# Kernel optimization log

Hardware: AMD Instinct MI355X
Metric: run time of the kernel (lower is better)

The kernel has to match this reference:

```python
import jax, jax.numpy as jnp
import numpy as np

N_NODES = 100000
N_EDGES = 1600000
NFEAT = 512
HIDDEN = 128
NCLASS = 40


def setup_inputs() -> dict:
    key = jax.random.key(0)
    ks = jax.random.split(key, 8)
    x = jax.random.normal(ks[0], (N_NODES, NFEAT), dtype=jnp.float32)
    edge_src = jax.random.randint(ks[1], (N_EDGES,), 0, N_NODES, dtype=jnp.int32)
    edge_dst = jax.random.randint(ks[2], (N_EDGES,), 0, N_NODES, dtype=jnp.int32)
    # normalized adjacency values (D^-1/2 A D^-1/2 style), all positive
    edge_val = jax.random.uniform(ks[3], (N_EDGES,), dtype=jnp.float32)
    # glorot-ish init like pygcn's reset_parameters
    W1 = jax.random.normal(ks[4], (NFEAT, HIDDEN), dtype=jnp.float32) / np.sqrt(NFEAT)
    b1 = jnp.zeros((HIDDEN,), dtype=jnp.float32)
    W2 = jax.random.normal(ks[5], (HIDDEN, NCLASS), dtype=jnp.float32) / np.sqrt(HIDDEN)
    b2 = jnp.zeros((NCLASS,), dtype=jnp.float32)
    return {"x": x, "edge_src": edge_src, "edge_dst": edge_dst, "edge_val": edge_val,
            "W1": W1, "b1": b1, "W2": W2, "b2": b2}


def _gcn_layer(h, edge_src, edge_dst, edge_val, W, b):
    # support = h @ W ; out = spmm(adj, support) + b
    support = h @ W                                  # [N, d_out]
    msg = support[edge_src] * edge_val[:, None]      # [E, d_out] gather
    agg = jax.ops.segment_sum(msg, edge_dst, num_segments=N_NODES)  # scatter-add
    return agg + b


def reference(x, edge_src, edge_dst, edge_val, W1, b1, W2, b2):
    h = _gcn_layer(x, edge_src, edge_dst, edge_val, W1, b1)
    h = jax.nn.relu(h)
    # dropout=0.0 -> branch skipped (faithful to `if self.dropout:` with falsy value)
    h = _gcn_layer(h, edge_src, edge_dst, edge_val, W2, b2)
    return jax.nn.log_softmax(h, axis=1)
```

## Files before the change

kernel.cpp:

```cpp
#include <hip/hip_runtime.h>
#include <stdint.h>

#define NN 100000
#define NE 1600000
#define NF 512
#define NH 128
#define NC 40
#define BKT 64

typedef float f32x4 __attribute__((ext_vector_type(4)));
typedef short bf16x8 __attribute__((ext_vector_type(8)));

__device__ __forceinline__ unsigned short f2bf(float f){
    unsigned u = __float_as_uint(f);
    u = u + 0x7FFFu + ((u >> 16) & 1u);
    return (unsigned short)(u >> 16);
}
__device__ __forceinline__ unsigned pk2(float a, float b){
    return (unsigned)f2bf(a) | ((unsigned)f2bf(b) << 16);
}
__device__ __forceinline__ float blo(unsigned u){ return __uint_as_float(u << 16); }
__device__ __forceinline__ float bhi(unsigned u){ return __uint_as_float(u & 0xffff0000u); }

__global__ __launch_bounds__(256) void edge_prep(const int* __restrict__ esrc,
                       const int* __restrict__ edst, const float* __restrict__ eval,
                       int* __restrict__ deg, int2* __restrict__ pk,
                       const float* __restrict__ W1, const float* __restrict__ W2,
                       unsigned short* __restrict__ W1t, unsigned short* __restrict__ W2t){
    if (blockIdx.x < 280){
        int tid = blockIdx.x * 256 + threadIdx.x;
        if (tid < NF * NH){
            int c = tid >> 9;
            int k = tid & 511;
            W1t[c * NF + k] = f2bf(W1[k * NH + c]);
        }
        int t2 = tid - NF * NH;
        if (t2 >= 0 && t2 < 48 * NH){
            int c = t2 >> 7;
            int k = t2 & 127;
            W2t[c * NH + k] = (c < NC) ? f2bf(W2[k * NC + c]) : (unsigned short)0;
        }
    } else {
        int tid = (blockIdx.x - 280) * 256 + threadIdx.x;
        if (tid < NE){
            int d = edst[tid];
            int pos = atomicAdd(&deg[d], 1);
            if (pos < BKT)
                pk[(size_t)d * BKT + pos] = make_int2(esrc[tid], __float_as_int(eval[tid]));
        }
    }
}

__global__ __launch_bounds__(256, 3) void gemm1(const float* __restrict__ x,
                                                const unsigned short* __restrict__ W1t,
                                                unsigned short* __restrict__ s1){
    __shared__ unsigned short Al[2][128 * 40];
    __shared__ unsigned short Bl[2][128 * 40];
    const int tid  = threadIdx.x;
    const int wid  = tid >> 6;
    const int lane = tid & 63;
    const int quad = lane >> 4;
    const int l15  = lane & 15;
    const int br   = blockIdx.x * 128;

    const int r    = tid >> 1;
    const int half = tid & 1;

    int arow = br + r; if (arow >= NN) arow = NN - 1;
    const float* aptr = x + (size_t)arow * NF + half * 16;
    const unsigned short* bptr = W1t + (size_t)r * NF + half * 16;

    float4 pa0, pa1, pa2, pa3;
    uint4  pb0, pb1;
    {
        const float4* ap = (const float4*)aptr;
        pa0 = ap[0]; pa1 = ap[1]; pa2 = ap[2]; pa3 = ap[3];
        const uint4* bp = (const uint4*)bptr;
        pb0 = bp[0]; pb1 = bp[1];
        unsigned* Ad = (unsigned*)&Al[0][r * 40 + half * 16];
        Ad[0] = pk2(pa0.x, pa0.y); Ad[1] = pk2(pa0.z, pa0.w);
        Ad[2] = pk2(pa1.x, pa1.y); Ad[3] = pk2(pa1.z, pa1.w);
        Ad[4] = pk2(pa2.x, pa2.y); Ad[5] = pk2(pa2.z, pa2.w);
        Ad[6] = pk2(pa3.x, pa3.y); Ad[7] = pk2(pa3.z, pa3.w);
        uint4* Bd = (uint4*)&Bl[0][r * 40 + half * 16];
        Bd[0] = pb0; Bd[1] = pb1;
    }
    __syncthreads();

    f32x4 acc[2][8];
#pragma unroll
    for (int i = 0; i < 2; i++)
#pragma unroll
        for (int j = 0; j < 8; j++) acc[i][j] = (f32x4){0.f, 0.f, 0.f, 0.f};

    int cur = 0;
    for (int ks = 0; ks < NF; ks += 32){
        const bool more = (ks + 32 < NF);
        if (more){
            const float4* ap = (const float4*)(aptr + ks + 32);
            pa0 = ap[0]; pa1 = ap[1]; pa2 = ap[2]; pa3 = ap[3];
            const uint4* bp = (const uint4*)(bptr + ks + 32);
            pb0 = bp[0]; pb1 = bp[1];
        }

        bf16x8 a0 = *(const bf16x8*)&Al[cur][(wid * 32 +      l15) * 40 + quad * 8];
        bf16x8 a1 = *(const bf16x8*)&Al[cur][(wid * 32 + 16 + l15) * 40 + quad * 8];
        bf16x8 bb[8];
#pragma unroll
        for (int ct = 0; ct < 8; ct++)
            bb[ct] = *(const bf16x8*)&Bl[cur][(ct * 16 + l15) * 40 + quad * 8];
#pragma unroll
        for (int ct = 0; ct < 8; ct++){
            acc[0][ct] = __builtin_amdgcn_mfma_f32_16x16x32_bf16(a0, bb[ct], acc[0][ct], 0, 0, 0);
            acc[1][ct] = __builtin_amdgcn_mfma_f32_16x16x32_bf16(a1, bb[ct], acc[1][ct], 0, 0, 0);
        }

        if (more){
            int nxt = cur ^ 1;
            unsigned* Ad = (unsigned*)&Al[nxt][r * 40 + half * 16];
            Ad[0] = pk2(pa0.x, pa0.y); Ad[1] = pk2(pa0.z, pa0.w);
            Ad[2] = pk2(pa1.x, pa1.y); Ad[3] = pk2(pa1.z, pa1.w);
            Ad[4] = pk2(pa2.x, pa2.y); Ad[5] = pk2(pa2.z, pa2.w);
            Ad[6] = pk2(pa3.x, pa3.y); Ad[7] = pk2(pa3.z, pa3.w);
            uint4* Bd = (uint4*)&Bl[nxt][r * 40 + half * 16];
            Bd[0] = pb0; Bd[1] = pb1;
        }
        __syncthreads();
        cur ^= 1;
    }

#pragma unroll
    for (int rt = 0; rt < 2; rt++)
#pragma unroll
        for (int ct = 0; ct < 8; ct++)
#pragma unroll
            for (int i = 0; i < 4; i++){
                int row = br + wid * 32 + rt * 16 + quad * 4 + i;
                if (row < NN) s1[(size_t)row * NH + ct * 16 + l15] = f2bf(acc[rt][ct][i]);
            }
}

__global__ __launch_bounds__(256) void agg1(const uint4* __restrict__ s1v,
                                            const int* __restrict__ deg,
                                            const int2* __restrict__ pk,
                                            const float* __restrict__ b1, uint4* __restrict__ h){
    const int lane  = threadIdx.x & 63;
    const int quad  = lane >> 4;
    const int hl    = lane & 15;
    const int lbase = quad * 16;
    const int node  = blockIdx.x * 16 + (threadIdx.x >> 6) * 4 + quad;

    const int s = node * BKT;
    int dg = deg[node]; if (dg > BKT) dg = BKT;
    const int e = s + dg;
    float a[8];
#pragma unroll
    for (int t = 0; t < 8; t++) a[t] = 0.f;

    int2 rec = make_int2(0, 0);
    {
        int c0 = e - s; if (c0 > 16) c0 = 16;
        if (hl < c0) rec = pk[s + hl];
    }
    for (int base = s; base < e; base += 16){
        int cnt = e - base; if (cnt > 16) cnt = 16;
        int2 cur = rec;
        int nb = base + 16;
        if (nb < e){
            int cn = e - nb; if (cn > 16) cn = 16;
            rec = make_int2(0, 0);
            if (hl < cn) rec = pk[nb + hl];
        }
        int j = 0;
        for (; j + 8 <= cnt; j += 8){
            int is[8];
#pragma unroll
            for (int q = 0; q < 8; q++) is[q] = __shfl(cur.x, lbase + j + q, 64);
            uint4 us[8];
#pragma unroll
            for (int q = 0; q < 8; q++) us[q] = s1v[(size_t)is[q] * 16 + hl];
            float vs[8];
#pragma unroll
            for (int q = 0; q < 8; q++) vs[q] = __int_as_float(__shfl(cur.y, lbase + j + q, 64));
#pragma unroll
            for (int q = 0; q < 8; q++){
                float v = vs[q];
                a[0] += v * blo(us[q].x); a[1] += v * bhi(us[q].x);
                a[2] += v * blo(us[q].y); a[3] += v * bhi(us[q].y);
                a[4] += v * blo(us[q].z); a[5] += v * bhi(us[q].z);
                a[6] += v * blo(us[q].w); a[7] += v * bhi(us[q].w);
            }
        }
        for (; j < cnt; j++){
            int   i0 = __shfl(cur.x, lbase + j, 64);
            float v0 = __int_as_float(__shfl(cur.y, lbase + j, 64));
            uint4 u  = s1v[(size_t)i0 * 16 + hl];
            a[0] += v0 * blo(u.x); a[1] += v0 * bhi(u.x);
            a[2] += v0 * blo(u.y); a[3] += v0 * bhi(u.y);
            a[4] += v0 * blo(u.z); a[5] += v0 * bhi(u.z);
            a[6] += v0 * blo(u.w); a[7] += v0 * bhi(u.w);
        }
    }
    const float4* b1v = (const float4*)b1;
    float4 bA = b1v[2 * hl], bB = b1v[2 * hl + 1];
    a[0] += bA.x; a[1] += bA.y; a[2] += bA.z; a[3] += bA.w;
    a[4] += bB.x; a[5] += bB.y; a[6] += bB.z; a[7] += bB.w;
#pragma unroll
    for (int t = 0; t < 8; t++) a[t] = fmaxf(a[t], 0.f);
    h[(size_t)node * 16 + hl] = make_uint4(pk2(a[0], a[1]), pk2(a[2], a[3]),
                                           pk2(a[4], a[5]), pk2(a[6], a[7]));
}

__global__ __launch_bounds__(256) void gemm2(const unsigned short* __restrict__ h,
                                             const unsigned short* __restrict__ W2t,
                                             unsigned short* __restrict__ s2p){
    const int tid  = threadIdx.x;
    const int wid  = tid >> 6;
    const int lane = tid & 63;
    const int quad = lane >> 4;
    const int l15  = lane & 15;
    const int row0 = blockIdx.x * 64 + wid * 16;

    bf16x8 bf[3][4];
#pragma unroll
    for (int ct = 0; ct < 3; ct++)
#pragma unroll
        for (int ks = 0; ks < 4; ks++)
            bf[ct][ks] = *(const bf16x8*)&W2t[(ct * 16 + l15) * NH + ks * 32 + quad * 8];

    int arow = row0 + l15; if (arow >= NN) arow = NN - 1;
    const unsigned short* ap = h + (size_t)arow * NH;

    bf16x8 a[4];
#pragma unroll
    for (int ks = 0; ks < 4; ks++) a[ks] = *(const bf16x8*)&ap[ks * 32 + quad * 8];

    f32x4 acc[3];
#pragma unroll
    for (int ct = 0; ct < 3; ct++) acc[ct] = (f32x4){0.f, 0.f, 0.f, 0.f};
#pragma unroll
    for (int ks = 0; ks < 4; ks++)
#pragma unroll
        for (int ct = 0; ct < 3; ct++)
            acc[ct] = __builtin_amdgcn_mfma_f32_16x16x32_bf16(a[ks], bf[ct][ks], acc[ct], 0, 0, 0);

#pragma unroll
    for (int ct = 0; ct < 3; ct++)
#pragma unroll
        for (int i = 0; i < 4; i++){
            int row = row0 + quad * 4 + i;
            if (row < NN) s2p[(size_t)row * 64 + ct * 16 + l15] = f2bf(acc[ct][i]);
        }
}

__global__ __launch_bounds__(256) void agg2(const uint4* __restrict__ s2v,
                                            const int* __restrict__ deg,
                                            const int2* __restrict__ pk,
                                            const float* __restrict__ b2, float* __restrict__ out){
    const int lane  = threadIdx.x & 63;
    const int oct   = lane >> 3;
    const int hl    = lane & 7;
    const int lbase = oct * 8;
    const int node  = blockIdx.x * 32 + (threadIdx.x >> 6) * 8 + oct;

    const int s = node * BKT;
    int dg = deg[node]; if (dg > BKT) dg = BKT;
    const int e = s + dg;
    float a[8];
#pragma unroll
    for (int t = 0; t < 8; t++) a[t] = 0.f;

    int2 rec = make_int2(0, 0);
    {
        int c0 = e - s; if (c0 > 8) c0 = 8;
        if (hl < c0) rec = pk[s + hl];
    }
    for (int base = s; base < e; base += 8){
        int cnt = e - base; if (cnt > 8) cnt = 8;
        int2 cur = rec;
        int nb = base + 8;
        if (nb < e){
            int cn = e - nb; if (cn > 8) cn = 8;
            rec = make_int2(0, 0);
            if (hl < cn) rec = pk[nb + hl];
        }
        if (cnt == 8){
            int is[8];
#pragma unroll
            for (int q = 0; q < 8; q++) is[q] = __shfl(cur.x, lbase + q, 64);
            uint4 us[8];
#pragma unroll
            for (int q = 0; q < 8; q++) us[q] = s2v[(size_t)is[q] * 8 + hl];
            float vs[8];
#pragma unroll
            for (int q = 0; q < 8; q++) vs[q] = __int_as_float(__shfl(cur.y, lbase + q, 64));
#pragma unroll
            for (int q = 0; q < 8; q++){
                float v = vs[q];
                a[0] += v * blo(us[q].x); a[1] += v * bhi(us[q].x);
                a[2] += v * blo(us[q].y); a[3] += v * bhi(us[q].y);
                a[4] += v * blo(us[q].z); a[5] += v * bhi(us[q].z);
                a[6] += v * blo(us[q].w); a[7] += v * bhi(us[q].w);
            }
        } else {
            for (int j = 0; j < cnt; j++){
                int   i0 = __shfl(cur.x, lbase + j, 64);
                float v0 = __int_as_float(__shfl(cur.y, lbase + j, 64));
                uint4 u  = s2v[(size_t)i0 * 8 + hl];
                a[0] += v0 * blo(u.x); a[1] += v0 * bhi(u.x);
                a[2] += v0 * blo(u.y); a[3] += v0 * bhi(u.y);
                a[4] += v0 * blo(u.z); a[5] += v0 * bhi(u.z);
                a[6] += v0 * blo(u.w); a[7] += v0 * bhi(u.w);
            }
        }
    }
    const bool act = hl < 5;
    float z[8];
    if (act){
        const float4* b2v = (const float4*)b2;
        float4 cA = b2v[2 * hl], cB = b2v[2 * hl + 1];
        z[0] = a[0] + cA.x; z[1] = a[1] + cA.y; z[2] = a[2] + cA.z; z[3] = a[3] + cA.w;
        z[4] = a[4] + cB.x; z[5] = a[5] + cB.y; z[6] = a[6] + cB.z; z[7] = a[7] + cB.w;
    } else {
#pragma unroll
        for (int t = 0; t < 8; t++) z[t] = -INFINITY;
    }
    float m = z[0];
#pragma unroll
    for (int t = 1; t < 8; t++) m = fmaxf(m, z[t]);
#pragma unroll
    for (int o = 4; o; o >>= 1) m = fmaxf(m, __shfl_xor(m, o, 8));
    float pe = 0.f;
    if (act){
#pragma unroll
        for (int t = 0; t < 8; t++) pe += __expf(z[t] - m);
    }
#pragma unroll
    for (int o = 4; o; o >>= 1) pe += __shfl_xor(pe, o, 8);
    if (act){
        float l = __logf(pe) + m;
        float* op = out + (size_t)node * NC + 8 * hl;
        *(float4*)op       = make_float4(z[0] - l, z[1] - l, z[2] - l, z[3] - l);
        *(float4*)(op + 4) = make_float4(z[4] - l, z[5] - l, z[6] - l, z[7] - l);
    }
}

extern "C" void kernel_launch(void* const* d_in, const int* in_sizes, int n_in,
                              void* d_out, int out_size, void* d_ws, size_t ws_size,
                              hipStream_t stream) {
    const float* x    = (const float*)d_in[0];
    const int*   esrc = (const int*)  d_in[1];
    const int*   edst = (const int*)  d_in[2];
    const float* eval = (const float*)d_in[3];
    const float* W1   = (const float*)d_in[4];
    const float* b1   = (const float*)d_in[5];
    const float* W2   = (const float*)d_in[6];
    const float* b2   = (const float*)d_in[7];
    float* out = (float*)d_out;

    char* ws = (char*)d_ws;
    size_t off = 0;
    auto alloc = [&](size_t bytes) -> void* {
        void* p = ws + off;
        off += (bytes + 255) & ~(size_t)255;
        return p;
    };
    unsigned short* W1t  = (unsigned short*)alloc((size_t)NF * NH * 2);
    unsigned short* W2t  = (unsigned short*)alloc((size_t)48 * NH * 2);
    unsigned short* s1   = (unsigned short*)alloc((size_t)NN * NH * 2);
    unsigned short* h    = (unsigned short*)alloc((size_t)NN * NH * 2);
    unsigned short* s2p  = (unsigned short*)alloc((size_t)NN * 64 * 2);
    int*   deg   = (int*)  alloc((size_t)NN * 4);
    int2*  pk    = (int2*) alloc((size_t)NN * BKT * 8);

    hipMemsetAsync(deg, 0, (size_t)NN * 4, stream);

    edge_prep<<<280 + (NE + 255) / 256, 256, 0, stream>>>(esrc, edst, eval, deg, pk, W1, W2, W1t, W2t);
    gemm1    <<<(NN + 127) / 128, 256, 0, stream>>>(x, W1t, s1);
    agg1     <<<NN / 16, 256, 0, stream>>>((const uint4*)s1, deg, pk, b1, (uint4*)h);
    gemm2    <<<(NN + 63) / 64, 256, 0, stream>>>(h, W2t, s2p);
    agg2     <<<NN / 32, 256, 0, stream>>>((const uint4*)s2p, deg, pk, b2, out);
}
```

Before: 551.9 us.

## Fuse edge bucketing into gemm1 launch and pad degree counters apart

Splits the weight transpose into its own small kernel and merges the edge bucketing blocks into the gemm1 launch as extra blocks, so the atomic-heavy edge scatter can overlap with the dense GEMM. Degree counters are spaced 16 ints apart (64 bytes) so that atomics to different nodes do not contend on the same cache line. In exchange the memset grows 16x (6.4 MB), agg kernels read deg with a strided pattern, and the GEMM blocks now share the device with edge blocks.

Result: faster. 501.6 us (-9.1%).

```diff
diff --git a/kernel.cpp b/kernel.cpp
--- a/kernel.cpp
+++ b/kernel.cpp
@@ -7,6 +7,8 @@
 #define NH 128
 #define NC 40
 #define BKT 64
+#define DEGS 16
+#define NGB 782
 
 typedef float f32x4 __attribute__((ext_vector_type(4)));
 typedef short bf16x8 __attribute__((ext_vector_type(8)));
@@ -22,40 +24,41 @@
 __device__ __forceinline__ float blo(unsigned u){ return __uint_as_float(u << 16); }
 __device__ __forceinline__ float bhi(unsigned u){ return __uint_as_float(u & 0xffff0000u); }
 
-__global__ __launch_bounds__(256) void edge_prep(const int* __restrict__ esrc,
-                       const int* __restrict__ edst, const float* __restrict__ eval,
-                       int* __restrict__ deg, int2* __restrict__ pk,
-                       const float* __restrict__ W1, const float* __restrict__ W2,
-                       unsigned short* __restrict__ W1t, unsigned short* __restrict__ W2t){
-    if (blockIdx.x < 280){
-        int tid = blockIdx.x * 256 + threadIdx.x;
-        if (tid < NF * NH){
-            int c = tid >> 9;
-            int k = tid & 511;
-            W1t[c * NF + k] = f2bf(W1[k * NH + c]);
-        }
-        int t2 = tid - NF * NH;
-        if (t2 >= 0 && t2 < 48 * NH){
-            int c = t2 >> 7;
-            int k = t2 & 127;
-            W2t[c * NH + k] = (c < NC) ? f2bf(W2[k * NC + c]) : (unsigned short)0;
-        }
-    } else {
-        int tid = (blockIdx.x - 280) * 256 + threadIdx.x;
+__global__ __launch_bounds__(256) void wprep(const float* __restrict__ W1, const float* __restrict__ W2,
+                                             unsigned short* __restrict__ W1t, unsigned short* __restrict__ W2t){
+    int tid = blockIdx.x * 256 + threadIdx.x;
+    if (tid < NF * NH){
+        int c = tid >> 9;
+        int k = tid & 511;
+        W1t[c * NF + k] = f2bf(W1[k * NH + c]);
+    }
+    int t2 = tid - NF * NH;
+    if (t2 >= 0 && t2 < 48 * NH){
+        int c = t2 >> 7;
+        int k = t2 & 127;
+        W2t[c * NH + k] = (c < NC) ? f2bf(W2[k * NC + c]) : (unsigned short)0;
+    }
+}
+
+__global__ __launch_bounds__(256, 3) void gemm1_edge(const float* __restrict__ x,
+                                                     const unsigned short* __restrict__ W1t,
+                                                     unsigned short* __restrict__ s1,
+                                                     const int* __restrict__ esrc,
+                                                     const int* __restrict__ edst,
+                                                     const float* __restrict__ eval,
+                                                     int* __restrict__ deg, int2* __restrict__ pk){
+    __shared__ unsigned short Al[2][128 * 40];
+    __shared__ unsigned short Bl[2][128 * 40];
+    if (blockIdx.x >= NGB){
+        int tid = (blockIdx.x - NGB) * 256 + threadIdx.x;
         if (tid < NE){
             int d = edst[tid];
-            int pos = atomicAdd(&deg[d], 1);
+            int pos = atomicAdd(&deg[d * DEGS], 1);
             if (pos < BKT)
                 pk[(size_t)d * BKT + pos] = make_int2(esrc[tid], __float_as_int(eval[tid]));
         }
-    }
-}
-
-__global__ __launch_bounds__(256, 3) void gemm1(const float* __restrict__ x,
-                                                const unsigned short* __restrict__ W1t,
-                                                unsigned short* __restrict__ s1){
-    __shared__ unsigned short Al[2][128 * 40];
-    __shared__ unsigned short Bl[2][128 * 40];
+        return;
+    }
     const int tid  = threadIdx.x;
     const int wid  = tid >> 6;
     const int lane = tid & 63;
@@ -151,7 +154,7 @@
     const int node  = blockIdx.x * 16 + (threadIdx.x >> 6) * 4 + quad;
 
     const int s = node * BKT;
-    int dg = deg[node]; if (dg > BKT) dg = BKT;
+    int dg = deg[node * DEGS]; if (dg > BKT) dg = BKT;
     const int e = s + dg;
     float a[8];
 #pragma unroll
@@ -264,7 +267,7 @@
     const int node  = blockIdx.x * 32 + (threadIdx.x >> 6) * 8 + oct;
 
     const int s = node * BKT;
-    int dg = deg[node]; if (dg > BKT) dg = BKT;
+    int dg = deg[node * DEGS]; if (dg > BKT) dg = BKT;
     const int e = s + dg;
     float a[8];
 #pragma unroll
@@ -370,14 +373,14 @@
     unsigned short* s1   = (unsigned short*)alloc((size_t)NN * NH * 2);
     unsigned short* h    = (unsigned short*)alloc((size_t)NN * NH * 2);
     unsigned short* s2p  = (unsigned short*)alloc((size_t)NN * 64 * 2);
-    int*   deg   = (int*)  alloc((size_t)NN * 4);
+    int*   deg   = (int*)  alloc((size_t)NN * DEGS * 4);
     int2*  pk    = (int2*) alloc((size_t)NN * BKT * 8);
 
-    hipMemsetAsync(deg, 0, (size_t)NN * 4, stream);
-
-    edge_prep<<<280 + (NE + 255) / 256, 256, 0, stream>>>(esrc, edst, eval, deg, pk, W1, W2, W1t, W2t);
-    gemm1    <<<(NN + 127) / 128, 256, 0, stream>>>(x, W1t, s1);
-    agg1     <<<NN / 16, 256, 0, stream>>>((const uint4*)s1, deg, pk, b1, (uint4*)h);
-    gemm2    <<<(NN + 63) / 64, 256, 0, stream>>>(h, W2t, s2p);
-    agg2     <<<NN / 32, 256, 0, stream>>>((const uint4*)s2p, deg, pk, b2, out);
-}
+    hipMemsetAsync(deg, 0, (size_t)NN * DEGS * 4, stream);
+
+    wprep     <<<280, 256, 0, stream>>>(W1, W2, W1t, W2t);
+    gemm1_edge<<<NGB + (NE + 255) / 256, 256, 0, stream>>>(x, W1t, s1, esrc, edst, eval, deg, pk);
+    agg1      <<<NN / 16, 256, 0, stream>>>((const uint4*)s1, deg, pk, b1, (uint4*)h);
+    gemm2     <<<(NN + 63) / 64, 256, 0, stream>>>(h, W2t, s2p);
+    agg2      <<<NN / 32, 256, 0, stream>>>((const uint4*)s2p, deg, pk, b2, out);
+}
```
